# Kernel optimization log

Hardware: AMD Instinct MI355X
Metric: run time of the kernel (lower is better)

Reference implementation:

```python
import jax, jax.numpy as jnp
import numpy as np

D = 768          # TGLU_hidden_dim == input_hidden_dim
E = 8            # num_experts
TOP_K = 2        # top_experts
N_ENT = 32       # num_entity
B = 16           # batch (mentions)
L = 128          # max_seq_len
EPS = 1e-5


def setup_inputs() -> dict:
    key = jax.random.key(0)
    ks = jax.random.split(key, 16)
    s = 0.02
    return {
        "entity_text_cls": jax.random.normal(ks[0], (N_ENT, D), jnp.float32),
        "entity_text_tokens": jax.random.normal(ks[1], (N_ENT, L, D), jnp.float32),
        "mention_text_cls": jax.random.normal(ks[2], (B, D), jnp.float32),
        "mention_text_tokens": jax.random.normal(ks[3], (B, L, D), jnp.float32),
        # SwitchMoE params: gate + per-expert Linear(dim -> output_dim)
        "gate_w": jax.random.normal(ks[4], (D, E), jnp.float32) * s,
        "gate_b": jnp.zeros((E,), jnp.float32),
        "exp_w": jax.random.normal(ks[5], (E, D, D), jnp.float32) * s,
        "exp_b": jnp.zeros((E, D), jnp.float32),
        # attention projections
        "wq": jax.random.normal(ks[6], (D, D), jnp.float32) * s,
        "bq": jnp.zeros((D,), jnp.float32),
        "wk": jax.random.normal(ks[7], (D, D), jnp.float32) * s,
        "bk": jnp.zeros((D,), jnp.float32),
        "wv": jax.random.normal(ks[8], (D, D), jnp.float32) * s,
        "bv": jnp.zeros((D,), jnp.float32),
        # LayerNorm params
        "ln_w": jnp.ones((D,), jnp.float32),
        "ln_b": jnp.zeros((D,), jnp.float32),
    }


def _switch_moe(x, gate_w, gate_b, exp_w, exp_b):
    # x: [n, s, D] -> [n, s, D]; top-k router, renormalized combine.
    logits = jnp.einsum("nsd,de->nse", x, gate_w) + gate_b
    probs = jax.nn.softmax(logits, axis=-1)
    vals, idx = jax.lax.top_k(probs, TOP_K)              # [n,s,k]
    vals = vals / jnp.sum(vals, axis=-1, keepdims=True)
    # combine weights over all experts (zero for unselected) -> dense mask form
    w = jnp.sum(jax.nn.one_hot(idx, E, dtype=x.dtype) * vals[..., None], axis=-2)  # [n,s,E]
    eo = jnp.einsum("nsd,edo->nseo", x, exp_w) + exp_b   # [n,s,E,D]
    return jnp.einsum("nse,nseo->nso", w, eo)


def _layernorm(x, w, b):
    mu = jnp.mean(x, axis=-1, keepdims=True)
    var = jnp.mean(jnp.square(x - mu), axis=-1, keepdims=True)
    return (x - mu) * jax.lax.rsqrt(var + EPS) * w + b


def reference(entity_text_cls, entity_text_tokens, mention_text_cls, mention_text_tokens,
              gate_w, gate_b, exp_w, exp_b, wq, bq, wk, bk, wv, bv, ln_w, ln_b):
    # prepend CLS, route through shared MoE
    ent = jnp.concatenate([entity_text_cls[:, None, :], entity_text_tokens], axis=1)   # [N,L+1,D]
    ent_moe = _switch_moe(ent, gate_w, gate_b, exp_w, exp_b)
    ent_cls_moe = ent_moe[:, 0, :]          # [N,D]
    ent_tok = ent_moe[:, 1:, :]             # [N,L,D]

    men = jnp.concatenate([mention_text_cls[:, None, :], mention_text_tokens], axis=1)  # [B,L+1,D]
    men_moe = _switch_moe(men, gate_w, gate_b, exp_w, exp_b)
    men_tok = men_moe[:, 1:, :]             # [B,L,D]

    q = jnp.einsum("nld,do->nlo", ent_tok, wq) + bq    # [N,L,D]
    k = jnp.einsum("bmd,do->bmo", men_tok, wk) + bk    # [B,L,D]
    v = jnp.einsum("bmd,do->bmo", men_tok, wv) + bv    # [B,L,D]

    # all-pairs entity x mention cross attention: [N,B,L,L]
    scores = jnp.einsum("nld,bmd->nblm", q, k) / jnp.sqrt(jnp.asarray(D, q.dtype))
    probs = jax.nn.softmax(scores, axis=-1)
    context = jnp.einsum("nblm,bmd->nbld", probs, v)   # [N,B,L,D]
    context = jnp.mean(context, axis=-2)               # [N,B,D]
    context = _layernorm(context, ln_w, ln_b)

    g2l = jnp.sum(ent_cls_moe[:, None, :] * context, axis=-1)   # [N,B]
    g2l = g2l.T                                                  # [B,N]
    g2g = mention_text_cls @ entity_text_cls.T                   # [B,N]
    return (g2l + g2g) / 2
```

## Files before the change

### kernel.cpp

```cpp
#include <hip/hip_runtime.h>
#include <math.h>

#define D 768
#define NE 8
#define NTOK 6192
#define MEN_TOK0 4128

typedef __attribute__((ext_vector_type(8))) short short8;
typedef __attribute__((ext_vector_type(4))) short short4b;
typedef __attribute__((ext_vector_type(4))) float floatx4;

__device__ __forceinline__ short f2bf(float f) {
  union { float f; unsigned u; } x; x.f = f;
  unsigned r = x.u + 0x7fffu + ((x.u >> 16) & 1u);
  return (short)(r >> 16);
}
__device__ __forceinline__ float bf2f(short s) {
  union { unsigned u; float f; } x; x.u = ((unsigned)(unsigned short)s) << 16;
  return x.f;
}

__device__ __forceinline__ void gload16(const short* g, short8* lds_base) {
  __builtin_amdgcn_global_load_lds(
      (const __attribute__((address_space(1))) unsigned int*)g,
      (__attribute__((address_space(3))) unsigned int*)lds_base,
      16, 0, 0);
}

#define PIPE_BAR(NSTR)                                            \
  do {                                                            \
    asm volatile("s_waitcnt vmcnt(" NSTR ")" ::: "memory");       \
    __builtin_amdgcn_sched_barrier(0);                            \
    __builtin_amdgcn_s_barrier();                                 \
    __builtin_amdgcn_sched_barrier(0);                            \
  } while (0)

__device__ __forceinline__ const float* token_row(int t,
    const float* __restrict__ ecls, const float* __restrict__ etok,
    const float* __restrict__ mcls, const float* __restrict__ mtok) {
  if (t < MEN_TOK0) {
    int n = t / 129, s = t - n * 129;
    return (s == 0) ? (ecls + n * D) : (etok + (size_t)(n * 128 + s - 1) * D);
  } else {
    int tm = t - MEN_TOK0;
    int b = tm / 129, s = tm - b * 129;
    return (s == 0) ? (mcls + b * D) : (mtok + (size_t)(b * 128 + s - 1) * D);
  }
}

__global__ __launch_bounds__(256) void prep_kernel(
    const float* __restrict__ ecls, const float* __restrict__ etok,
    const float* __restrict__ mcls, const float* __restrict__ mtok,
    const float* __restrict__ gate_w, const float* __restrict__ gate_b,
    const float* __restrict__ exp_w, const float* __restrict__ wq,
    const float* __restrict__ wk, const float* __restrict__ wv,
    int* __restrict__ te1, int* __restrict__ te2,
    float* __restrict__ tw1, float* __restrict__ tw2,
    short* __restrict__ Xb, short* __restrict__ expwT, short* __restrict__ wT) {
  __shared__ float tbuf[64][65];
  int bid = blockIdx.x;
  int tid = threadIdx.x;
  if (bid < 1548) {
    int t = bid * 4 + (tid >> 6);
    int lane = tid & 63;
    const float* xr = token_row(t, ecls, etok, mcls, mtok);
    float acc[NE];
#pragma unroll
    for (int e = 0; e < NE; ++e) acc[e] = 0.f;
#pragma unroll
    for (int it = 0; it < 3; ++it) {
      int d0 = lane * 4 + it * 256;
      floatx4 x = *(const floatx4*)(xr + d0);
      short4b xb;
#pragma unroll
      for (int q = 0; q < 4; ++q) {
        xb[q] = f2bf(x[q]);
        float xv = x[q];
#pragma unroll
        for (int e = 0; e < NE; ++e) acc[e] += xv * gate_w[(d0 + q) * NE + e];
      }
      *(short4b*)(Xb + (size_t)t * D + d0) = xb;
    }
#pragma unroll
    for (int e = 0; e < NE; ++e) {
#pragma unroll
      for (int off = 32; off > 0; off >>= 1) acc[e] += __shfl_down(acc[e], off);
    }
    if (lane == 0) {
      float lg[NE];
#pragma unroll
      for (int e = 0; e < NE; ++e) lg[e] = acc[e] + gate_b[e];
      int e1 = 0;
#pragma unroll
      for (int e = 1; e < NE; ++e) if (lg[e] > lg[e1]) e1 = e;
      int e2 = (e1 == 0) ? 1 : 0;
#pragma unroll
      for (int e = 0; e < NE; ++e) {
        if (e != e1 && lg[e] > lg[e2]) e2 = e;
      }
      float w1 = 1.f / (1.f + __expf(lg[e2] - lg[e1]));
      te1[t] = e1; te2[t] = e2;
      tw1[t] = w1; tw2[t] = 1.f - w1;
    }
  } else {
    int zz = bid - 1548;
    int z = zz / 144, rem = zz % 144;
    int k0 = (rem / 12) * 64, o0 = (rem % 12) * 64;
    const float* src; short* dst;
    if (z < 8) { src = exp_w + (size_t)z * D * D; dst = expwT + (size_t)z * D * D; }
    else { src = (z == 8) ? wq : (z == 9) ? wk : wv; dst = wT + (size_t)(z - 8) * D * D; }
    int tx = tid & 63, ty = tid >> 6;
#pragma unroll
    for (int i = 0; i < 16; ++i) {
      int k = i * 4 + ty;
      tbuf[k][tx] = src[(size_t)(k0 + k) * D + o0 + tx];
    }
    __syncthreads();
#pragma unroll
    for (int i = 0; i < 16; ++i) {
      int o = i * 4 + ty;
      dst[(size_t)(o0 + o) * D + k0 + tx] = f2bf(tbuf[tx][o]);
    }
  }
}

__global__ __launch_bounds__(1024) void route_kernel(
    const int* __restrict__ te1, const int* __restrict__ te2,
    int* __restrict__ lst_tok, int* __restrict__ slot1, int* __restrict__ slot2,
    int* __restrict__ cnt, int* __restrict__ basee) {
  __shared__ int hist[NE];
  __shared__ int base_s[NE];
  int tid = threadIdx.x;
  if (tid < NE) hist[tid] = 0;
  __syncthreads();
  for (int t = tid; t < NTOK; t += 1024) {
    atomicAdd(&hist[te1[t]], 1);
    atomicAdd(&hist[te2[t]], 1);
  }
  __syncthreads();
  if (tid == 0) {
    int acc = 0;
    for (int e = 0; e < NE; ++e) {
      base_s[e] = acc;
      cnt[e] = hist[e];
      basee[e] = acc;
      acc += hist[e];
    }
  }
  __syncthreads();
  if (tid < NE) hist[tid] = 0;
  __syncthreads();
  for (int t = tid; t < NTOK; t += 1024) {
    int e1 = te1[t], e2 = te2[t];
    int r1 = atomicAdd(&hist[e1], 1);
    int r2 = atomicAdd(&hist[e2], 1);
    int s1 = base_s[e1] + r1;
    int s2 = base_s[e2] + r2;
    slot1[t] = s1; slot2[t] = s2;
    lst_tok[s1] = t; lst_tok[s2] = t;
  }
}

__global__ __launch_bounds__(512, 4) void moe_kernel(
    const short* __restrict__ Xb, const short* __restrict__ expwT,
    const int* __restrict__ cnt, const int* __restrict__ basee,
    const int* __restrict__ lst_tok, short* __restrict__ EO) {
  int id = blockIdx.x;
  int e = id & 7;
  int r = id >> 3;
  int ob = r % 6;
  int tb = r / 6;
  int count = cnt[e];
  int t0 = tb * 128;
  if (t0 >= count) return;
  int o0 = ob * 128;
  int gb = basee[e];

  __shared__ short8 As[1536];
  __shared__ short8 Bs[1536];
  __shared__ int stok[128];

  int tid = threadIdx.x;
  int l = tid & 63, w = tid >> 6;
  int wr = w >> 1, wc = w & 1;

  if (tid < 128) {
    int p = t0 + tid;
    stok[tid] = lst_tok[gb + (p < count ? p : 0)];
  }
  __syncthreads();

  const short* Bg = expwT + (size_t)e * D * D;
  int srow = tid >> 2, scc = tid & 3;
  int csrc = (scc ^ ((srow >> 1) & 3)) * 8;
  const short* srcA = Xb + (size_t)stok[srow] * D + csrc;
  const short* srcB = Bg + (size_t)(o0 + srow) * D + csrc;

  floatx4 acc[2][4];
#pragma unroll
  for (int ai = 0; ai < 2; ++ai)
#pragma unroll
    for (int bj = 0; bj < 4; ++bj) acc[ai][bj] = (floatx4){0.f, 0.f, 0.f, 0.f};

  gload16(srcA, &As[w << 6]);
  gload16(srcB, &Bs[w << 6]);
  gload16(srcA + 32, &As[512 + (w << 6)]);
  gload16(srcB + 32, &Bs[512 + (w << 6)]);

  for (int it = 0; it < 24; ++it) {
    if (it < 23) PIPE_BAR("2"); else PIPE_BAR("0");
    int cur = (it % 3) << 9;
    if (it < 22) {
      int nb = ((it + 2) % 3) << 9;
      int k0n = (it + 2) * 32;
      gload16(srcA + k0n, &As[nb + (w << 6)]);
      gload16(srcB + k0n, &Bs[nb + (w << 6)]);
    }
    int kc = l >> 4;
    short8 a[2], bb[4];
#pragma unroll
    for (int ai = 0; ai < 2; ++ai) {
      int ar = wr * 32 + ai * 16 + (l & 15);
      a[ai] = As[cur + (ar << 2) + (kc ^ ((ar >> 1) & 3))];
    }
#pragma unroll
    for (int bj = 0; bj < 4; ++bj) {
      int br = wc * 64 + bj * 16 + (l & 15);
      bb[bj] = Bs[cur + (br << 2) + (kc ^ ((br >> 1) & 3))];
    }
#pragma unroll
    for (int ai = 0; ai < 2; ++ai)
#pragma unroll
      for (int bj = 0; bj < 4; ++bj)
        acc[ai][bj] = __builtin_amdgcn_mfma_f32_16x16x32_bf16(a[ai], bb[bj], acc[ai][bj], 0, 0, 0);
  }

#pragma unroll
  for (int ai = 0; ai < 2; ++ai) {
#pragma unroll
    for (int rr = 0; rr < 4; ++rr) {
      int rowl = wr * 32 + ai * 16 + ((l >> 4) << 2) + rr;
      int p = t0 + rowl;
      if (p < count) {
        size_t off = (size_t)(gb + p) * D;
#pragma unroll
        for (int bj = 0; bj < 4; ++bj) {
          int col = o0 + wc * 64 + bj * 16 + (l & 15);
          EO[off + col] = f2bf(acc[ai][bj][rr]);
        }
      }
    }
  }
}

__global__ __launch_bounds__(256) void combine_kernel(
    const short* __restrict__ EO,
    const int* __restrict__ te1, const int* __restrict__ te2,
    const float* __restrict__ tw1, const float* __restrict__ tw2,
    const int* __restrict__ slot1, const int* __restrict__ slot2,
    const float* __restrict__ exp_b, short* __restrict__ MOEb) {
  int idx = blockIdx.x * 256 + threadIdx.x;
  int t = idx / 96, cg = idx - t * 96;
  int c0 = cg * 8;
  int e1 = te1[t], e2 = te2[t];
  float w1 = tw1[t], w2 = tw2[t];
  short8 a = *(const short8*)(EO + (size_t)slot1[t] * D + c0);
  short8 b = *(const short8*)(EO + (size_t)slot2[t] * D + c0);
  const float* b1 = exp_b + e1 * D + c0;
  const float* b2 = exp_b + e2 * D + c0;
  short8 o;
#pragma unroll
  for (int j = 0; j < 8; ++j)
    o[j] = f2bf(w1 * (bf2f(a[j]) + b1[j]) + w2 * (bf2f(b[j]) + b2[j]));
  *(short8*)(MOEb + (size_t)t * D + c0) = o;
}

__global__ __launch_bounds__(512, 4) void qkv_kernel(
    const short* __restrict__ MOEb, const short* __restrict__ wT,
    const float* __restrict__ bq, const float* __restrict__ bk,
    const float* __restrict__ bv,
    short* __restrict__ Qb, short* __restrict__ Kb, short* __restrict__ Vb) {
  int id = blockIdx.x;
  int z, r;
  if (id < 384)      { z = 0; r = id; }
  else if (id < 576) { z = 1; r = id - 384; }
  else               { z = 2; r = id - 576; }
  int tb = r / 6, ob = r % 6;
  int o0 = ob * 128;
  int base = (z == 0) ? 0 : MEN_TOK0;
  const short* W = wT + (size_t)z * D * D;
  const float* bias = (z == 0) ? bq : (z == 1) ? bk : bv;
  int tokbase = base + (tb >> 1) * 129 + 1 + (tb & 1) * 64;
  const short* Ag = MOEb + (size_t)tokbase * D;

  __shared__ short8 As[768];
  __shared__ short8 Bs[1536];

  int tid = threadIdx.x;
  int l = tid & 63, w = tid >> 6;
  int wr = w >> 1, wc = w & 1;

  int srow = tid >> 2, scc = tid & 3;
  int csrc = (scc ^ ((srow >> 1) & 3)) * 8;
  const short* srcA = Ag + (size_t)(srow & 63) * D + csrc;
  const short* srcB = W + (size_t)(o0 + srow) * D + csrc;

  floatx4 acc[4];
#pragma unroll
  for (int bj = 0; bj < 4; ++bj) acc[bj] = (floatx4){0.f, 0.f, 0.f, 0.f};

  if (w < 4) gload16(srcA, &As[w << 6]);
  gload16(srcB, &Bs[w << 6]);
  if (w < 4) gload16(srcA + 32, &As[256 + (w << 6)]);
  gload16(srcB + 32, &Bs[512 + (w << 6)]);

  for (int it = 0; it < 24; ++it) {
    if (it < 23) {
      if (w < 4) {
        asm volatile("s_waitcnt vmcnt(2)" ::: "memory");
      } else {
        asm volatile("s_waitcnt vmcnt(1)" ::: "memory");
      }
    } else {
      asm volatile("s_waitcnt vmcnt(0)" ::: "memory");
    }
    __builtin_amdgcn_sched_barrier(0);
    __builtin_amdgcn_s_barrier();
    __builtin_amdgcn_sched_barrier(0);

    int curA = (it % 3) << 8;
    int curB = (it % 3) << 9;
    if (it < 22) {
      int nb = (it + 2) % 3;
      int k0n = (it + 2) * 32;
      if (w < 4) gload16(srcA + k0n, &As[(nb << 8) + (w << 6)]);
      gload16(srcB + k0n, &Bs[(nb << 9) + (w << 6)]);
    }
    int kc = l >> 4;
    int ar = wr * 16 + (l & 15);
    short8 a = As[curA + (ar << 2) + (kc ^ ((ar >> 1) & 3))];
    short8 bb[4];
#pragma unroll
    for (int bj = 0; bj < 4; ++bj) {
      int br = wc * 64 + bj * 16 + (l & 15);
      bb[bj] = Bs[curB + (br << 2) + (kc ^ ((br >> 1) & 3))];
    }
#pragma unroll
    for (int bj = 0; bj < 4; ++bj)
      acc[bj] = __builtin_amdgcn_mfma_f32_16x16x32_bf16(a, bb[bj], acc[bj], 0, 0, 0);
  }

#pragma unroll
  for (int rr = 0; rr < 4; ++rr) {
    int rowl = wr * 16 + ((l >> 4) << 2) + rr;
    size_t rglob = (size_t)tb * 64 + rowl;
#pragma unroll
    for (int bj = 0; bj < 4; ++bj) {
      int col = o0 + wc * 64 + bj * 16 + (l & 15);
      float v = acc[bj][rr] + bias[col];
      if (z == 0)      Qb[rglob * D + col] = f2bf(v);
      else if (z == 1) Kb[rglob * D + col] = f2bf(v);
      else             Vb[rglob * D + col] = f2bf(v);
    }
  }
}

__device__ __forceinline__ float blockSum512(float v, volatile float* red, int tid) {
#pragma unroll
  for (int off = 32; off > 0; off >>= 1) v += __shfl_down(v, off);
  __syncthreads();
  if ((tid & 63) == 0) red[tid >> 6] = v;
  __syncthreads();
  float s = 0.f;
#pragma unroll
  for (int i = 0; i < 8; ++i) s += red[i];
  return s;
}

__global__ __launch_bounds__(512, 4) void attn_kernel(
    const short* __restrict__ Qb, const short* __restrict__ Kb,
    const short* __restrict__ Vb, const short* __restrict__ MOEb,
    const float* __restrict__ ecls, const float* __restrict__ mcls,
    const float* __restrict__ ln_w, const float* __restrict__ ln_b,
    float* __restrict__ out) {
  int id = blockIdx.x;
  int n = id & 31, b = id >> 5;
  __shared__ short8 Qs[1536];
  __shared__ short8 Ks[1536];
  __shared__ float pb[128];
  __shared__ float red[8];
  int tid = threadIdx.x;
  int l = tid & 63, w = tid >> 6;
  if (tid < 128) pb[tid] = 0.f;
  __syncthreads();

  floatx4 acc[8];
#pragma unroll
  for (int j = 0; j < 8; ++j) acc[j] = (floatx4){0.f, 0.f, 0.f, 0.f};

  const short* qg = Qb + (size_t)n * 128 * D;
  const short* kg = Kb + (size_t)b * 128 * D;

  int srow = tid >> 2, scc = tid & 3;
  int csrc = (scc ^ ((srow >> 1) & 3)) * 8;
  const short* srcQ = qg + (size_t)srow * D + csrc;
  const short* srcK = kg + (size_t)srow * D + csrc;

  gload16(srcQ, &Qs[w << 6]);
  gload16(srcK, &Ks[w << 6]);
  gload16(srcQ + 32, &Qs[512 + (w << 6)]);
  gload16(srcK + 32, &Ks[512 + (w << 6)]);

  for (int it = 0; it < 24; ++it) {
    if (it < 23) PIPE_BAR("2"); else PIPE_BAR("0");
    int cur = (it % 3) << 9;
    if (it < 22) {
      int nb = ((it + 2) % 3) << 9;
      int k0n = (it + 2) * 32;
      gload16(srcQ + k0n, &Qs[nb + (w << 6)]);
      gload16(srcK + k0n, &Ks[nb + (w << 6)]);
    }
    int kc = l >> 4;
    int ar = w * 16 + (l & 15);
    short8 a = Qs[cur + (ar << 2) + (kc ^ ((ar >> 1) & 3))];
    short8 bb[8];
#pragma unroll
    for (int j = 0; j < 8; ++j) {
      int br = j * 16 + (l & 15);
      bb[j] = Ks[cur + (br << 2) + (kc ^ ((br >> 1) & 3))];
    }
#pragma unroll
    for (int j = 0; j < 8; ++j)
      acc[j] = __builtin_amdgcn_mfma_f32_16x16x32_bf16(a, bb[j], acc[j], 0, 0, 0);
  }

  const float scale = 0.03608439182435161f;
  float colsum[8];
#pragma unroll
  for (int j = 0; j < 8; ++j) colsum[j] = 0.f;

#pragma unroll
  for (int r = 0; r < 4; ++r) {
    float mx = -3.0e38f;
#pragma unroll
    for (int j = 0; j < 8; ++j) mx = fmaxf(mx, acc[j][r]);
    mx = fmaxf(mx, __shfl_xor(mx, 1));
    mx = fmaxf(mx, __shfl_xor(mx, 2));
    mx = fmaxf(mx, __shfl_xor(mx, 4));
    mx = fmaxf(mx, __shfl_xor(mx, 8));
    float pv[8], sm = 0.f;
#pragma unroll
    for (int j = 0; j < 8; ++j) { pv[j] = __expf((acc[j][r] - mx) * scale); sm += pv[j]; }
    sm += __shfl_xor(sm, 1);
    sm += __shfl_xor(sm, 2);
    sm += __shfl_xor(sm, 4);
    sm += __shfl_xor(sm, 8);
    float inv = 1.f / sm;
#pragma unroll
    for (int j = 0; j < 8; ++j) colsum[j] += pv[j] * inv;
  }
#pragma unroll
  for (int j = 0; j < 8; ++j) {
    colsum[j] += __shfl_xor(colsum[j], 16);
    colsum[j] += __shfl_xor(colsum[j], 32);
  }
  if (l < 16) {
#pragma unroll
    for (int j = 0; j < 8; ++j) atomicAdd(&pb[j * 16 + l], colsum[j]);
  }
  __syncthreads();

  float ctx[4] = {0.f, 0.f, 0.f, 0.f};
  bool act = tid < 192;
  int d0 = tid << 2;
  if (act) {
    const short* vb = Vb + (size_t)b * 128 * D + d0;
    for (int m = 0; m < 128; ++m) {
      float p = pb[m];
      short4b v = *(const short4b*)(vb + (size_t)m * D);
#pragma unroll
      for (int j = 0; j < 4; ++j) ctx[j] += p * bf2f(v[j]);
    }
#pragma unroll
    for (int j = 0; j < 4; ++j) ctx[j] *= (1.f / 128.f);
  }

  float mu = blockSum512(ctx[0] + ctx[1] + ctx[2] + ctx[3], red, tid) * (1.f / 768.f);
  float c[4];
#pragma unroll
  for (int j = 0; j < 4; ++j) c[j] = ctx[j] - mu;
  float vs = act ? (c[0]*c[0] + c[1]*c[1] + c[2]*c[2] + c[3]*c[3]) : 0.f;
  float var = blockSum512(vs, red, tid) * (1.f / 768.f);
  float rstd = rsqrtf(var + 1e-5f);

  float g2l_p = 0.f, g2g_p = 0.f;
  if (act) {
    floatx4 lw = *(const floatx4*)(ln_w + d0);
    floatx4 lb = *(const floatx4*)(ln_b + d0);
    short4b em = *(const short4b*)(MOEb + (size_t)(n * 129) * D + d0);
    floatx4 mc = *(const floatx4*)(mcls + (size_t)b * D + d0);
    floatx4 ec = *(const floatx4*)(ecls + (size_t)n * D + d0);
#pragma unroll
    for (int j = 0; j < 4; ++j) {
      float cl = c[j] * rstd * lw[j] + lb[j];
      g2l_p += bf2f(em[j]) * cl;
      g2g_p += mc[j] * ec[j];
    }
  }
  float g2l = blockSum512(g2l_p, red, tid);
  float g2g = blockSum512(g2g_p, red, tid);
  if (tid == 0) out[b * 32 + n] = 0.5f * (g2l + g2g);
}

extern "C" void kernel_launch(void* const* d_in, const int* in_sizes, int n_in,
                              void* d_out, int out_size, void* d_ws, size_t ws_size,
                              hipStream_t stream) {
  const float* ecls   = (const float*)d_in[0];
  const float* etok   = (const float*)d_in[1];
  const float* mcls   = (const float*)d_in[2];
  const float* mtok   = (const float*)d_in[3];
  const float* gate_w = (const float*)d_in[4];
  const float* gate_b = (const float*)d_in[5];
  const float* exp_w  = (const float*)d_in[6];
  const float* exp_b  = (const float*)d_in[7];
  const float* wq     = (const float*)d_in[8];
  const float* bq     = (const float*)d_in[9];
  const float* wk     = (const float*)d_in[10];
  const float* bk     = (const float*)d_in[11];
  const float* wv     = (const float*)d_in[12];
  const float* bv     = (const float*)d_in[13];
  const float* ln_w   = (const float*)d_in[14];
  const float* ln_b   = (const float*)d_in[15];
  float* outp = (float*)d_out;

  char* ws = (char*)d_ws;
  short* Qb    = (short*)(ws + 0);
  short* Kb    = (short*)(ws + 6291456);
  short* Vb    = (short*)(ws + 9437184);
  short* Xb    = (short*)(ws + 12582912);
  short* EO    = (short*)(ws + 22093824);
  short* MOEb  = (short*)(ws + 41115648);
  short* expwT = (short*)(ws + 50626560);
  short* wT    = (short*)(ws + 60063744);
  int*   te1   = (int*)  (ws + 63602688);
  int*   te2   = (int*)  (ws + 63627456);
  float* tw1   = (float*)(ws + 63652224);
  float* tw2   = (float*)(ws + 63676992);
  int*   slot1 = (int*)  (ws + 63701760);
  int*   slot2 = (int*)  (ws + 63726528);
  int*   lst_tok = (int*)(ws + 63751296);
  int*   cnt   = (int*)  (ws + 63800832);
  int*   basee = (int*)  (ws + 63800864);

  prep_kernel<<<1548 + 1584, 256, 0, stream>>>(ecls, etok, mcls, mtok, gate_w, gate_b,
                                               exp_w, wq, wk, wv,
                                               te1, te2, tw1, tw2, Xb, expwT, wT);
  route_kernel<<<1, 1024, 0, stream>>>(te1, te2, lst_tok, slot1, slot2, cnt, basee);
  moe_kernel<<<49 * 6 * 8, 512, 0, stream>>>(Xb, expwT, cnt, basee, lst_tok, EO);
  combine_kernel<<<2322, 256, 0, stream>>>(EO, te1, te2, tw1, tw2, slot1, slot2,
                                           exp_b, MOEb);
  qkv_kernel<<<768, 512, 0, stream>>>(MOEb, wT, bq, bk, bv, Qb, Kb, Vb);
  attn_kernel<<<512, 512, 0, stream>>>(Qb, Kb, Vb, MOEb, ecls, mcls, ln_w, ln_b, outp);
}
```

Before: 121.3 us.

## Use 2x4 MFMA warp tiling in QKV and attention score GEMMs

After: 121.8 us. No clear change (+0.5%).

```diff
diff --git a/kernel.cpp b/kernel.cpp
--- a/kernel.cpp
+++ b/kernel.cpp
@@ -282,18 +282,17 @@
     short* __restrict__ Qb, short* __restrict__ Kb, short* __restrict__ Vb) {
   int id = blockIdx.x;
   int z, r;
-  if (id < 384)      { z = 0; r = id; }
-  else if (id < 576) { z = 1; r = id - 384; }
-  else               { z = 2; r = id - 576; }
+  if (id < 192)      { z = 0; r = id; }
+  else if (id < 288) { z = 1; r = id - 192; }
+  else               { z = 2; r = id - 288; }
   int tb = r / 6, ob = r % 6;
   int o0 = ob * 128;
   int base = (z == 0) ? 0 : MEN_TOK0;
   const short* W = wT + (size_t)z * D * D;
   const float* bias = (z == 0) ? bq : (z == 1) ? bk : bv;
-  int tokbase = base + (tb >> 1) * 129 + 1 + (tb & 1) * 64;
-  const short* Ag = MOEb + (size_t)tokbase * D;
-
-  __shared__ short8 As[768];
+  const short* Ag = MOEb + (size_t)(base + tb * 129 + 1) * D;
+
+  __shared__ short8 As[1536];
   __shared__ short8 Bs[1536];
 
   int tid = threadIdx.x;
@@ -302,65 +301,62 @@
 
   int srow = tid >> 2, scc = tid & 3;
   int csrc = (scc ^ ((srow >> 1) & 3)) * 8;
-  const short* srcA = Ag + (size_t)(srow & 63) * D + csrc;
+  const short* srcA = Ag + (size_t)srow * D + csrc;
   const short* srcB = W + (size_t)(o0 + srow) * D + csrc;
 
-  floatx4 acc[4];
-#pragma unroll
-  for (int bj = 0; bj < 4; ++bj) acc[bj] = (floatx4){0.f, 0.f, 0.f, 0.f};
-
-  if (w < 4) gload16(srcA, &As[w << 6]);
+  floatx4 acc[2][4];
+#pragma unroll
+  for (int ai = 0; ai < 2; ++ai)
+#pragma unroll
+    for (int bj = 0; bj < 4; ++bj) acc[ai][bj] = (floatx4){0.f, 0.f, 0.f, 0.f};
+
+  gload16(srcA, &As[w << 6]);
   gload16(srcB, &Bs[w << 6]);
-  if (w < 4) gload16(srcA + 32, &As[256 + (w << 6)]);
+  gload16(srcA + 32, &As[512 + (w << 6)]);
   gload16(srcB + 32, &Bs[512 + (w << 6)]);
 
   for (int it = 0; it < 24; ++it) {
-    if (it < 23) {
-      if (w < 4) {
-        asm volatile("s_waitcnt vmcnt(2)" ::: "memory");
-      } else {
-        asm volatile("s_waitcnt vmcnt(1)" ::: "memory");
-      }
-    } else {
-      asm volatile("s_waitcnt vmcnt(0)" ::: "memory");
-    }
-    __builtin_amdgcn_sched_barrier(0);
-    __builtin_amdgcn_s_barrier();
-    __builtin_amdgcn_sched_barrier(0);
-
-    int curA = (it % 3) << 8;
-    int curB = (it % 3) << 9;
+    if (it < 23) PIPE_BAR("2"); else PIPE_BAR("0");
+    int cur = (it % 3) << 9;
     if (it < 22) {
-      int nb = (it + 2) % 3;
+      int nb = ((it + 2) % 3) << 9;
       int k0n = (it + 2) * 32;
-      if (w < 4) gload16(srcA + k0n, &As[(nb << 8) + (w << 6)]);
-      gload16(srcB + k0n, &Bs[(nb << 9) + (w << 6)]);
+      gload16(srcA + k0n, &As[nb + (w << 6)]);
+      gload16(srcB + k0n, &Bs[nb + (w << 6)]);
     }
     int kc = l >> 4;
-    int ar = wr * 16 + (l & 15);
-    short8 a = As[curA + (ar << 2) + (kc ^ ((ar >> 1) & 3))];
-    short8 bb[4];
+    short8 a[2], bb[4];
+#pragma unroll
+    for (int ai = 0; ai < 2; ++ai) {
+      int ar = wr * 32 + ai * 16 + (l & 15);
+      a[ai] = As[cur + (ar << 2) + (kc ^ ((ar >> 1) & 3))];
+    }
 #pragma unroll
     for (int bj = 0; bj < 4; ++bj) {
       int br = wc * 64 + bj * 16 + (l & 15);
-      bb[bj] = Bs[curB + (br << 2) + (kc ^ ((br >> 1) & 3))];
-    }
-#pragma unroll
-    for (int bj = 0; bj < 4; ++bj)
-      acc[bj] = __builtin_amdgcn_mfma_f32_16x16x32_bf16(a, bb[bj], acc[bj], 0, 0, 0);
-  }
-
-#pragma unroll
-  for (int rr = 0; rr < 4; ++rr) {
-    int rowl = wr * 16 + ((l >> 4) << 2) + rr;
-    size_t rglob = (size_t)tb * 64 + rowl;
-#pragma unroll
-    for (int bj = 0; bj < 4; ++bj) {
-      int col = o0 + wc * 64 + bj * 16 + (l & 15);
-      float v = acc[bj][rr] + bias[col];
-      if (z == 0)      Qb[rglob * D + col] = f2bf(v);
-      else if (z == 1) Kb[rglob * D + col] = f2bf(v);
-      else             Vb[rglob * D + col] = f2bf(v);
+      bb[bj] = Bs[cur + (br << 2) + (kc ^ ((br >> 1) & 3))];
+    }
+#pragma unroll
+    for (int ai = 0; ai < 2; ++ai)
+#pragma unroll
+      for (int bj = 0; bj < 4; ++bj)
+        acc[ai][bj] = __builtin_amdgcn_mfma_f32_16x16x32_bf16(a[ai], bb[bj], acc[ai][bj], 0, 0, 0);
+  }
+
+#pragma unroll
+  for (int ai = 0; ai < 2; ++ai) {
+#pragma unroll
+    for (int rr = 0; rr < 4; ++rr) {
+      int rowl = wr * 32 + ai * 16 + ((l >> 4) << 2) + rr;
+      size_t rglob = (size_t)tb * 128 + rowl;
+#pragma unroll
+      for (int bj = 0; bj < 4; ++bj) {
+        int col = o0 + wc * 64 + bj * 16 + (l & 15);
+        float v = acc[ai][bj][rr] + bias[col];
+        if (z == 0)      Qb[rglob * D + col] = f2bf(v);
+        else if (z == 1) Kb[rglob * D + col] = f2bf(v);
+        else             Vb[rglob * D + col] = f2bf(v);
+      }
     }
   }
 }
@@ -389,14 +385,19 @@
   __shared__ short8 Ks[1536];
   __shared__ float pb[128];
   __shared__ float red[8];
+  float* smm = (float*)Qs;
+  float* sss = (float*)Qs + 256;
   int tid = threadIdx.x;
   int l = tid & 63, w = tid >> 6;
+  int wr = w >> 1, wc = w & 1;
   if (tid < 128) pb[tid] = 0.f;
   __syncthreads();
 
-  floatx4 acc[8];
-#pragma unroll
-  for (int j = 0; j < 8; ++j) acc[j] = (floatx4){0.f, 0.f, 0.f, 0.f};
+  floatx4 acc[2][4];
+#pragma unroll
+  for (int ai = 0; ai < 2; ++ai)
+#pragma unroll
+    for (int bj = 0; bj < 4; ++bj) acc[ai][bj] = (floatx4){0.f, 0.f, 0.f, 0.f};
 
   const short* qg = Qb + (size_t)n * 128 * D;
   const short* kg = Kb + (size_t)b * 128 * D;
@@ -421,52 +422,91 @@
       gload16(srcK + k0n, &Ks[nb + (w << 6)]);
     }
     int kc = l >> 4;
-    int ar = w * 16 + (l & 15);
-    short8 a = Qs[cur + (ar << 2) + (kc ^ ((ar >> 1) & 3))];
-    short8 bb[8];
-#pragma unroll
-    for (int j = 0; j < 8; ++j) {
-      int br = j * 16 + (l & 15);
-      bb[j] = Ks[cur + (br << 2) + (kc ^ ((br >> 1) & 3))];
-    }
-#pragma unroll
-    for (int j = 0; j < 8; ++j)
-      acc[j] = __builtin_amdgcn_mfma_f32_16x16x32_bf16(a, bb[j], acc[j], 0, 0, 0);
+    short8 a[2], bb[4];
+#pragma unroll
+    for (int ai = 0; ai < 2; ++ai) {
+      int ar = wr * 32 + ai * 16 + (l & 15);
+      a[ai] = Qs[cur + (ar << 2) + (kc ^ ((ar >> 1) & 3))];
+    }
+#pragma unroll
+    for (int bj = 0; bj < 4; ++bj) {
+      int br = wc * 64 + bj * 16 + (l & 15);
+      bb[bj] = Ks[cur + (br << 2) + (kc ^ ((br >> 1) & 3))];
+    }
+#pragma unroll
+    for (int ai = 0; ai < 2; ++ai)
+#pragma unroll
+      for (int bj = 0; bj < 4; ++bj)
+        acc[ai][bj] = __builtin_amdgcn_mfma_f32_16x16x32_bf16(a[ai], bb[bj], acc[ai][bj], 0, 0, 0);
   }
 
   const float scale = 0.03608439182435161f;
-  float colsum[8];
-#pragma unroll
-  for (int j = 0; j < 8; ++j) colsum[j] = 0.f;
-
-#pragma unroll
-  for (int r = 0; r < 4; ++r) {
-    float mx = -3.0e38f;
-#pragma unroll
-    for (int j = 0; j < 8; ++j) mx = fmaxf(mx, acc[j][r]);
-    mx = fmaxf(mx, __shfl_xor(mx, 1));
-    mx = fmaxf(mx, __shfl_xor(mx, 2));
-    mx = fmaxf(mx, __shfl_xor(mx, 4));
-    mx = fmaxf(mx, __shfl_xor(mx, 8));
-    float pv[8], sm = 0.f;
-#pragma unroll
-    for (int j = 0; j < 8; ++j) { pv[j] = __expf((acc[j][r] - mx) * scale); sm += pv[j]; }
-    sm += __shfl_xor(sm, 1);
-    sm += __shfl_xor(sm, 2);
-    sm += __shfl_xor(sm, 4);
-    sm += __shfl_xor(sm, 8);
-    float inv = 1.f / sm;
-#pragma unroll
-    for (int j = 0; j < 8; ++j) colsum[j] += pv[j] * inv;
-  }
-#pragma unroll
-  for (int j = 0; j < 8; ++j) {
-    colsum[j] += __shfl_xor(colsum[j], 16);
-    colsum[j] += __shfl_xor(colsum[j], 32);
+  float mloc[2][4], sloc[2][4];
+#pragma unroll
+  for (int ai = 0; ai < 2; ++ai) {
+#pragma unroll
+    for (int r = 0; r < 4; ++r) {
+      float mx = -3.0e38f;
+#pragma unroll
+      for (int bj = 0; bj < 4; ++bj) mx = fmaxf(mx, acc[ai][bj][r]);
+      mx = fmaxf(mx, __shfl_xor(mx, 1));
+      mx = fmaxf(mx, __shfl_xor(mx, 2));
+      mx = fmaxf(mx, __shfl_xor(mx, 4));
+      mx = fmaxf(mx, __shfl_xor(mx, 8));
+      float sm = 0.f;
+#pragma unroll
+      for (int bj = 0; bj < 4; ++bj) {
+        float pv = __expf((acc[ai][bj][r] - mx) * scale);
+        acc[ai][bj][r] = pv;
+        sm += pv;
+      }
+      sm += __shfl_xor(sm, 1);
+      sm += __shfl_xor(sm, 2);
+      sm += __shfl_xor(sm, 4);
+      sm += __shfl_xor(sm, 8);
+      mloc[ai][r] = mx;
+      sloc[ai][r] = sm;
+    }
+  }
+  __syncthreads();
+  if ((l & 15) == 0) {
+#pragma unroll
+    for (int ai = 0; ai < 2; ++ai)
+#pragma unroll
+      for (int r = 0; r < 4; ++r) {
+        int row = wr * 32 + ai * 16 + ((l >> 4) << 2) + r;
+        smm[row * 2 + wc] = mloc[ai][r];
+        sss[row * 2 + wc] = sloc[ai][r];
+      }
+  }
+  __syncthreads();
+
+  float colsum[4];
+#pragma unroll
+  for (int bj = 0; bj < 4; ++bj) colsum[bj] = 0.f;
+#pragma unroll
+  for (int ai = 0; ai < 2; ++ai) {
+#pragma unroll
+    for (int r = 0; r < 4; ++r) {
+      int row = wr * 32 + ai * 16 + ((l >> 4) << 2) + r;
+      float m0 = smm[row * 2], m1 = smm[row * 2 + 1];
+      float s0 = sss[row * 2], s1 = sss[row * 2 + 1];
+      float M = fmaxf(m0, m1);
+      float Z = s0 * __expf((m0 - M) * scale) + s1 * __expf((m1 - M) * scale);
+      float fac = __expf((mloc[ai][r] - M) * scale) / Z;
+#pragma unroll
+      for (int bj = 0; bj < 4; ++bj) colsum[bj] += acc[ai][bj][r] * fac;
+    }
+  }
+#pragma unroll
+  for (int bj = 0; bj < 4; ++bj) {
+    colsum[bj] += __shfl_xor(colsum[bj], 16);
+    colsum[bj] += __shfl_xor(colsum[bj], 32);
   }
   if (l < 16) {
 #pragma unroll
-    for (int j = 0; j < 8; ++j) atomicAdd(&pb[j * 16 + l], colsum[j]);
+    for (int bj = 0; bj < 4; ++bj)
+      atomicAdd(&pb[wc * 64 + bj * 16 + l], colsum[bj]);
   }
   __syncthreads();
 
@@ -559,6 +599,6 @@
   moe_kernel<<<49 * 6 * 8, 512, 0, stream>>>(Xb, expwT, cnt, basee, lst_tok, EO);
   combine_kernel<<<2322, 256, 0, stream>>>(EO, te1, te2, tw1, tw2, slot1, slot2,
                                            exp_b, MOEb);
-  qkv_kernel<<<768, 512, 0, stream>>>(MOEb, wT, bq, bk, bv, Qb, Kb, Vb);
+  qkv_kernel<<<384, 512, 0, stream>>>(MOEb, wT, bq, bk, bv, Qb, Kb, Vb);
   attn_kernel<<<512, 512, 0, stream>>>(Qb, Kb, Vb, MOEb, ecls, mcls, ln_w, ln_b, outp);
 }
```
